# Optimization experiments

Measured on AMD Instinct MI355X. Metric: run time of the kernel, lower is better.

Reference implementation:

```python
import jax, jax.numpy as jnp
import numpy as np

M = 5  # neighbours per down point (M_i = 5 when n_up > 5)


def _per_graph(h, s_l, scores, W_emb, b_emb):
    # h: [N,H], s_l: [N,3], scores: [N]
    N, H = h.shape
    n_up = N // 4  # floor(0.25 * N)
    top_idx = jnp.argsort(-scores)[:n_up]
    up_mask = jnp.zeros((N,), bool).at[top_idx].set(True)
    up_idx = jnp.sort(top_idx)                     # up nodes in ascending node order
    down_idx = jnp.argsort(up_mask)[: N - n_up]    # stable: down nodes ascending

    # embedding_features_to_att: Linear(H+4 -> H) on concat(h, s_l, scores)
    feat = jnp.concatenate([h, s_l, scores[:, None]], axis=1) @ W_emb + b_emb  # [N,H]

    # directional KNN: for each down point, M nearest up points in 3D coords
    d2 = jnp.sum((s_l[down_idx][:, None, :] - s_l[up_idx][None, :, :]) ** 2, -1)  # [Nd,Nu]
    _, nn_local = jax.lax.top_k(-d2, M)            # [Nd,M] indices into up set
    dst = up_idx[nn_local].reshape(-1)             # edge destinations (up nodes)
    src = jnp.repeat(down_idx, M)                  # edge sources (down nodes)

    # DGL update_all: copy src 'features' -> max reduce at dst; no-msg nodes = 0
    msgs = feat[src]                               # [Nd*M, H]
    out = jnp.full((N, H), -jnp.inf, feat.dtype).at[dst].max(msgs)
    out = jnp.where(jnp.isneginf(out), jnp.zeros((), feat.dtype), out)
    return out, up_mask


def setup_inputs() -> dict:
    key = jax.random.key(0)
    k1, k2, k3, k4, k5 = jax.random.split(key, 5)
    B, N, H = 8, 8192, 256
    return {
        "h": jax.random.normal(k1, (B, N, H), jnp.float32),
        "s_l": jax.random.normal(k2, (B, N, 3), jnp.float32),
        "scores": jax.random.uniform(k3, (B, N), jnp.float32),
        "W_emb": jax.random.normal(k4, (H + 4, H), jnp.float32) * 0.02,
        "b_emb": jax.random.normal(k5, (H,), jnp.float32) * 0.02,
    }


def reference(h, s_l, scores, W_emb, b_emb):
    out, up_mask = jax.vmap(_per_graph, in_axes=(0, 0, 0, None, None))(
        h, s_l, scores, W_emb, b_emb)
    B, N, H = out.shape
    return out.reshape(B * N, H), up_mask.reshape(-1)
```

## Files before the change

kernel.cpp:

```cpp
#include <hip/hip_runtime.h>

#define Bb 8
#define Nn 8192
#define Hh 256
#define NUP 2048
#define NDOWN (Nn - NUP)
#define MM 5
#define EPB (NDOWN * MM)
#define KP 288
#define LDA 36
#define LSTW 17

typedef short v8s __attribute__((ext_vector_type(8)));
typedef float v4f __attribute__((ext_vector_type(4)));

__device__ __forceinline__ unsigned short bfc(float f) {
    unsigned u = __float_as_uint(f);
    return (unsigned short)((u + 0x7FFFu + ((u >> 16) & 1u)) >> 16);
}

template <int NB>
__device__ void find_kth_bin(const int* hist, int kth, int tid,
                             int* wsumA, int* res, int* out_bin, int* out_cntgt) {
    constexpr int PER = NB / 1024;
    int ln = tid & 63, wv = tid >> 6;
    int b0 = NB - 1 - PER * tid;
    int c0 = hist[b0];
    int c1 = (PER == 2) ? hist[b0 - 1] : 0;
    int tot = c0 + c1;
    int x = tot;
    #pragma unroll
    for (int off = 1; off < 64; off <<= 1) {
        int y = __shfl_up(x, off);
        if (ln >= off) x += y;
    }
    if (ln == 63) wsumA[wv] = x;
    __syncthreads();
    int wbase = 0;
    for (int w = 0; w < wv; w++) wbase += wsumA[w];
    int excl = wbase + x - tot;
    if (excl < kth && excl + c0 >= kth) { res[0] = b0; res[1] = excl; }
    else if (PER == 2 && excl + c0 < kth && excl + c0 + c1 >= kth) { res[0] = b0 - 1; res[1] = excl + c0; }
    __syncthreads();
    *out_bin = res[0];
    *out_cntgt = res[1];
}

__global__ __launch_bounds__(1024) void select_kernel(
        const float* __restrict__ scores, const float* __restrict__ sl,
        int* __restrict__ mask, float4* __restrict__ upc,
        float4* __restrict__ dnc, int* __restrict__ deg) {
    int b = blockIdx.x;
    int tid = threadIdx.x;
    int ln = tid & 63, wv = tid >> 6;
    __shared__ int hist[2048];
    __shared__ int wsumA[16], wsumB[16];
    __shared__ int res[2];
    __shared__ int sbase[2];
    const float* s = scores + (size_t)b * Nn;

    deg[b * NUP + tid] = 0;
    deg[b * NUP + 1024 + tid] = 0;

    hist[tid] = 0; hist[tid + 1024] = 0;
    __syncthreads();
    for (int t = tid; t < Nn; t += 1024)
        atomicAdd(&hist[__float_as_uint(s[t]) >> 21], 1);
    __syncthreads();
    int B1, gt1;
    find_kth_bin<2048>(hist, NUP, tid, wsumA, res, &B1, &gt1);
    int slots1 = NUP - gt1;

    hist[tid] = 0; hist[tid + 1024] = 0;
    __syncthreads();
    for (int t = tid; t < Nn; t += 1024) {
        unsigned u = __float_as_uint(s[t]);
        if ((int)(u >> 21) == B1) atomicAdd(&hist[(u >> 10) & 0x7FF], 1);
    }
    __syncthreads();
    int B2, gt2;
    find_kth_bin<2048>(hist, slots1, tid, wsumA, res, &B2, &gt2);
    int slots2 = slots1 - gt2;
    unsigned hi22 = ((unsigned)B1 << 11) | (unsigned)B2;

    hist[tid] = 0; hist[tid + 1024] = 0;
    __syncthreads();
    for (int t = tid; t < Nn; t += 1024) {
        unsigned u = __float_as_uint(s[t]);
        if ((u >> 10) == hi22) atomicAdd(&hist[u & 0x3FF], 1);
    }
    __syncthreads();
    int B3, gt3;
    find_kth_bin<1024>(hist, slots2, tid, wsumA, res, &B3, &gt3);
    int slots_eq = slots2 - gt3;
    unsigned T = (hi22 << 10) | (unsigned)B3;

    if (tid == 0) { sbase[0] = 0; sbase[1] = 0; }
    __syncthreads();
    for (int t0 = 0; t0 < Nn; t0 += 1024) {
        int node = t0 + tid;
        int g = b * Nn + node;
        unsigned u = __float_as_uint(s[node]);
        bool eq = (u == T);
        unsigned long long bal = __ballot(eq);
        unsigned long long lmask = (1ull << ln) - 1ull;
        int pre = __popcll(bal & lmask);
        if (ln == 0) wsumA[wv] = __popcll(bal);
        __syncthreads();
        int eqbase = sbase[0];
        for (int w = 0; w < wv; w++) eqbase += wsumA[w];
        bool up = (u > T) || (eq && (eqbase + pre) < slots_eq);
        unsigned long long bal2 = __ballot(up);
        int pre2 = __popcll(bal2 & lmask);
        if (ln == 0) wsumB[wv] = __popcll(bal2);
        __syncthreads();
        int upbase = sbase[1];
        for (int w = 0; w < wv; w++) upbase += wsumB[w];
        float4 c;
        c.x = sl[(size_t)g * 3 + 0];
        c.y = sl[(size_t)g * 3 + 1];
        c.z = sl[(size_t)g * 3 + 2];
        c.w = __int_as_float(node);
        if (up) {
            upc[b * NUP + upbase + pre2] = c;
        } else {
            dnc[b * NDOWN + node - (upbase + pre2)] = c;
        }
        mask[g] = up ? 1 : 0;
        __syncthreads();
        if (tid == 0) {
            int se = 0, su = 0;
            for (int w = 0; w < 16; w++) { se += wsumA[w]; su += wsumB[w]; }
            sbase[0] += se; sbase[1] += su;
        }
        __syncthreads();
    }
}

__global__ __launch_bounds__(512) void knn_brute(
        const float4* __restrict__ upc, const float4* __restrict__ dnc,
        int* __restrict__ knn, int* __restrict__ deg) {
    int b = blockIdx.y;
    int tid = threadIdx.x;
    int sub = tid >> 6, dn = tid & 63;
    __shared__ float xs[NUP], ys[NUP], zs[NUP];
    __shared__ unsigned long long Ubuf[1312];
    __shared__ int lcnt[64];
    float* sF = (float*)Ubuf;
    unsigned long long* lst = Ubuf + 32;

    float4 d = dnc[b * NDOWN + blockIdx.x * 64 + dn];
    float xd = d.x, yd = d.y, zd = d.z;
    int node = __float_as_int(d.w);

    const float4* U = upc + b * NUP;
    #pragma unroll
    for (int q = 0; q < 4; q++) {
        int i = q * 512 + tid;
        float4 u = U[i];
        xs[i] = u.x; ys[i] = u.y; zs[i] = u.z;
    }
    if (tid < 64) lcnt[tid] = 0;
    __syncthreads();

    float L[MM];
    #pragma unroll
    for (int m = 0; m < MM; m++) L[m] = 3.4e38f;
    const int j0 = sub * 256;
    #pragma unroll 4
    for (int j = j0; j < j0 + 256; ++j) {
        float dx = xs[j] - xd, dy = ys[j] - yd, dz = zs[j] - zd;
        float d2 = fmaf(dx, dx, fmaf(dy, dy, dz * dz));
        #pragma unroll
        for (int m = 0; m < MM; m++) {
            float lo = fminf(d2, L[m]), hi = fmaxf(d2, L[m]);
            L[m] = lo; d2 = hi;
        }
    }
    #pragma unroll
    for (int m = 0; m < MM; m++) sF[(sub * MM + m) * 64 + dn] = L[m];
    __syncthreads();

    if (sub == 0) {
        float F[MM];
        #pragma unroll
        for (int m = 0; m < MM; m++) F[m] = 3.4e38f;
        for (int l = 0; l < 8; l++) {
            #pragma unroll
            for (int m = 0; m < MM; m++) {
                float v = sF[(l * MM + m) * 64 + dn];
                #pragma unroll
                for (int k = 0; k < MM; k++) {
                    float lo = fminf(v, F[k]), hi = fmaxf(v, F[k]);
                    F[k] = lo; v = hi;
                }
            }
        }
        sF[dn] = F[MM - 1];
    }
    __syncthreads();
    float thr = sF[dn];

    #pragma unroll 4
    for (int j = j0; j < j0 + 256; ++j) {
        float dx = xs[j] - xd, dy = ys[j] - yd, dz = zs[j] - zd;
        float d2 = fmaf(dx, dx, fmaf(dy, dy, dz * dz));
        if (d2 <= thr) {
            unsigned long long key =
                ((unsigned long long)__float_as_uint(d2) << 32) |
                (unsigned long long)(unsigned)j;
            int s = atomicAdd(&lcnt[dn], 1);
            if (s < LSTW - 1) lst[dn * LSTW + s] = key;
        }
    }
    __syncthreads();

    if (sub == 0) {
        unsigned long long fin[MM];
        #pragma unroll
        for (int m = 0; m < MM; m++) fin[m] = 0xFFFFFFFFFFFFFFFFull;
        int n = min(lcnt[dn], LSTW - 1);
        for (int s = 0; s < n; s++) {
            unsigned long long cand = lst[dn * LSTW + s];
            #pragma unroll
            for (int m = 0; m < MM; m++) {
                bool lt = cand < fin[m];
                unsigned long long lo = lt ? cand : fin[m];
                unsigned long long hi = lt ? fin[m] : cand;
                fin[m] = lo; cand = hi;
            }
        }
        int g = b * Nn + node;
        #pragma unroll
        for (int m = 0; m < MM; m++) {
            int lid = (int)(unsigned)(fin[m] & 0xFFFFFFFFull);
            knn[g * MM + m] = lid;
            atomicAdd(&deg[b * NUP + lid], 1);
        }
    }
}

__global__ void wt_kernel(const float* __restrict__ W, const float* __restrict__ bias,
                          unsigned short* __restrict__ Wt) {
    int n = blockIdx.x;
    int k = threadIdx.x;
    Wt[n * KP + k] = bfc(W[(size_t)k * Hh + n]);
    if (k < KP - 256) {
        int kk = 256 + k;
        unsigned short v = 0;
        if (kk < 260)       v = bfc(W[(size_t)kk * Hh + n]);
        else if (kk == 260) v = bfc(bias[n]);
        Wt[n * KP + kk] = v;
    }
}

__global__ void feat_mfma(const float* __restrict__ h, const float* __restrict__ sl,
                          const float* __restrict__ sc, const unsigned short* __restrict__ Wt,
                          const float4* __restrict__ dnc, float* __restrict__ out) {
    int b = blockIdx.z;
    int m0 = blockIdx.x * 128;
    int n0 = blockIdx.y * 128;
    int tid = threadIdx.x;
    __shared__ unsigned short Al[128 * LDA];
    __shared__ unsigned short Bl[128 * LDA];
    __shared__ int ndid[128];
    int wid = tid >> 6, lane = tid & 63;
    int wm = (wid & 1) * 64, wn = (wid >> 1) * 64;
    int lm = lane & 15, quad = lane >> 4;
    if (tid < 128) ndid[tid] = __float_as_int(dnc[b * NDOWN + m0 + tid].w);
    v4f acc[4][4];
    #pragma unroll
    for (int i = 0; i < 4; i++)
        #pragma unroll
        for (int j = 0; j < 4; j++)
            acc[i][j] = (v4f){0.f, 0.f, 0.f, 0.f};
    const float* hb = h + (size_t)b * Nn * Hh;
    for (int t = 0; t < 9; t++) {
        int k0 = t * 32;
        __syncthreads();
        if (t < 8) {
            #pragma unroll
            for (int q = 0; q < 4; q++) {
                int e = q * 256 + tid;
                int row = e >> 3, kq = e & 7;
                float4 v = *(const float4*)(hb + (size_t)ndid[row] * Hh + k0 + kq * 4);
                ushort4 o = make_ushort4(bfc(v.x), bfc(v.y), bfc(v.z), bfc(v.w));
                *(ushort4*)(Al + row * LDA + kq * 4) = o;
            }
        } else if (tid < 128) {
            int row = tid;
            int g = b * Nn + ndid[row];
            unsigned short r[32];
            #pragma unroll
            for (int k = 0; k < 32; k++) r[k] = 0;
            r[0] = bfc(sl[(size_t)g * 3 + 0]);
            r[1] = bfc(sl[(size_t)g * 3 + 1]);
            r[2] = bfc(sl[(size_t)g * 3 + 2]);
            r[3] = bfc(sc[g]);
            r[4] = 0x3F80;
            #pragma unroll
            for (int q = 0; q < 8; q++)
                *(ushort4*)(Al + row * LDA + q * 4) =
                    make_ushort4(r[q * 4], r[q * 4 + 1], r[q * 4 + 2], r[q * 4 + 3]);
        }
        #pragma unroll
        for (int q = 0; q < 4; q++) {
            int e = q * 256 + tid;
            int n = e >> 3, kq = e & 7;
            ushort4 v = *(const ushort4*)(Wt + (size_t)(n0 + n) * KP + k0 + kq * 4);
            *(ushort4*)(Bl + n * LDA + kq * 4) = v;
        }
        __syncthreads();
        v8s af[4], bfr[4];
        #pragma unroll
        for (int i = 0; i < 4; i++)
            af[i] = *(const v8s*)(Al + (wm + i * 16 + lm) * LDA + quad * 8);
        #pragma unroll
        for (int j = 0; j < 4; j++)
            bfr[j] = *(const v8s*)(Bl + (wn + j * 16 + lm) * LDA + quad * 8);
        #pragma unroll
        for (int i = 0; i < 4; i++)
            #pragma unroll
            for (int j = 0; j < 4; j++)
                acc[i][j] = __builtin_amdgcn_mfma_f32_16x16x32_bf16(af[i], bfr[j], acc[i][j], 0, 0, 0);
    }
    #pragma unroll
    for (int i = 0; i < 4; i++) {
        #pragma unroll
        for (int r = 0; r < 4; r++) {
            int lrow = wm + i * 16 + quad * 4 + r;
            size_t base = ((size_t)b * Nn + ndid[lrow]) * Hh + n0 + wn + lm;
            #pragma unroll
            for (int j = 0; j < 4; j++)
                out[base + j * 16] = acc[i][j][r];
        }
    }
}

__global__ __launch_bounds__(1024) void csr_scan(const int* __restrict__ deg,
                                                 int* __restrict__ rowptr,
                                                 int* __restrict__ cursor) {
    int b = blockIdx.x;
    int tid = threadIdx.x;
    int ln = tid & 63, wv = tid >> 6;
    __shared__ int wsum[16];
    int d0 = deg[b * NUP + 2 * tid], d1 = deg[b * NUP + 2 * tid + 1];
    int s = d0 + d1;
    int x = s;
    #pragma unroll
    for (int off = 1; off < 64; off <<= 1) {
        int y = __shfl_up(x, off);
        if (ln >= off) x += y;
    }
    if (ln == 63) wsum[wv] = x;
    __syncthreads();
    int base = 0;
    for (int w = 0; w < wv; w++) base += wsum[w];
    int excl = base + x - s;
    rowptr[b * (NUP + 1) + 2 * tid] = excl;
    rowptr[b * (NUP + 1) + 2 * tid + 1] = excl + d0;
    cursor[b * NUP + 2 * tid] = excl;
    cursor[b * NUP + 2 * tid + 1] = excl + d0;
    if (tid == 1023) rowptr[b * (NUP + 1) + NUP] = excl + s;
}

__global__ void csr_fill(const int* __restrict__ mask, const int* __restrict__ knn,
                         int* __restrict__ cursor, int* __restrict__ edges) {
    int b = blockIdx.y;
    int i = blockIdx.x * 256 + threadIdx.x;
    int g = b * Nn + i;
    if (mask[g]) return;
    #pragma unroll
    for (int m = 0; m < MM; m++) {
        int un = knn[g * MM + m];
        int slot = atomicAdd(&cursor[b * NUP + un], 1);
        edges[b * EPB + slot] = i;
    }
}

__global__ void gather_kernel(const float4* __restrict__ upc, const int* __restrict__ rowptr,
                              const int* __restrict__ edges, float* __restrict__ out) {
    int b = blockIdx.y;
    int u = blockIdx.x * 4 + (threadIdx.x >> 6);
    int lane = threadIdx.x & 63;
    int node = __float_as_int(upc[b * NUP + u].w);
    int start = rowptr[b * (NUP + 1) + u];
    int end   = rowptr[b * (NUP + 1) + u + 1];
    const int* eb = edges + b * EPB;
    size_t rowbase = (size_t)b * Nn * Hh + (size_t)(lane << 2);
    float4 a0 = make_float4(-3.4e38f, -3.4e38f, -3.4e38f, -3.4e38f);
    float4 a1 = a0, a2 = a0, a3 = a0;
    int e = start;
    for (; e + 4 <= end; e += 4) {
        int s0 = eb[e], s1 = eb[e + 1], s2 = eb[e + 2], s3 = eb[e + 3];
        float4 v0 = *(const float4*)(out + rowbase + (size_t)s0 * Hh);
        float4 v1 = *(const float4*)(out + rowbase + (size_t)s1 * Hh);
        float4 v2 = *(const float4*)(out + rowbase + (size_t)s2 * Hh);
        float4 v3 = *(const float4*)(out + rowbase + (size_t)s3 * Hh);
        a0.x = fmaxf(a0.x, v0.x); a0.y = fmaxf(a0.y, v0.y);
        a0.z = fmaxf(a0.z, v0.z); a0.w = fmaxf(a0.w, v0.w);
        a1.x = fmaxf(a1.x, v1.x); a1.y = fmaxf(a1.y, v1.y);
        a1.z = fmaxf(a1.z, v1.z); a1.w = fmaxf(a1.w, v1.w);
        a2.x = fmaxf(a2.x, v2.x); a2.y = fmaxf(a2.y, v2.y);
        a2.z = fmaxf(a2.z, v2.z); a2.w = fmaxf(a2.w, v2.w);
        a3.x = fmaxf(a3.x, v3.x); a3.y = fmaxf(a3.y, v3.y);
        a3.z = fmaxf(a3.z, v3.z); a3.w = fmaxf(a3.w, v3.w);
    }
    for (; e < end; e++) {
        int s0 = eb[e];
        float4 v0 = *(const float4*)(out + rowbase + (size_t)s0 * Hh);
        a0.x = fmaxf(a0.x, v0.x); a0.y = fmaxf(a0.y, v0.y);
        a0.z = fmaxf(a0.z, v0.z); a0.w = fmaxf(a0.w, v0.w);
    }
    float4 r;
    r.x = fmaxf(fmaxf(a0.x, a1.x), fmaxf(a2.x, a3.x));
    r.y = fmaxf(fmaxf(a0.y, a1.y), fmaxf(a2.y, a3.y));
    r.z = fmaxf(fmaxf(a0.z, a1.z), fmaxf(a2.z, a3.z));
    r.w = fmaxf(fmaxf(a0.w, a1.w), fmaxf(a2.w, a3.w));
    if (start == end) r = make_float4(0.f, 0.f, 0.f, 0.f);
    *(float4*)(out + rowbase + (size_t)node * Hh) = r;
}

__global__ void finalize_kernel(const int* __restrict__ mask, float* __restrict__ out) {
    int b = blockIdx.y;
    int node = blockIdx.x * 4 + (threadIdx.x >> 6);
    int g = b * Nn + node;
    int lane = threadIdx.x & 63;
    bool up = mask[g] != 0;
    if (!up)
        *(float4*)(out + (size_t)g * Hh + (lane << 2)) = make_float4(0.f, 0.f, 0.f, 0.f);
    if (lane == 0) out[(size_t)Bb * Nn * Hh + g] = up ? 1.0f : 0.0f;
}

extern "C" void kernel_launch(void* const* d_in, const int* in_sizes, int n_in,
                              void* d_out, int out_size, void* d_ws, size_t ws_size,
                              hipStream_t stream) {
    const float* h    = (const float*)d_in[0];
    const float* sl   = (const float*)d_in[1];
    const float* sc   = (const float*)d_in[2];
    const float* W    = (const float*)d_in[3];
    const float* bias = (const float*)d_in[4];

    char* ws = (char*)d_ws;
    int* mask = (int*)ws;                 ws += (size_t)Bb * Nn * sizeof(int);
    int* knn  = (int*)ws;                 ws += (size_t)Bb * Nn * MM * sizeof(int);
    float4* upc = (float4*)ws;            ws += (size_t)Bb * NUP * sizeof(float4);
    float4* dnc = (float4*)ws;            ws += (size_t)Bb * NDOWN * sizeof(float4);
    unsigned short* Wt = (unsigned short*)ws; ws += (size_t)Hh * KP * sizeof(unsigned short);
    int* deg = (int*)ws;                  ws += (size_t)Bb * NUP * sizeof(int);
    int* cursor = (int*)ws;               ws += (size_t)Bb * NUP * sizeof(int);
    int* rowptr = (int*)ws;               ws += (size_t)Bb * (NUP + 1) * sizeof(int);
    int* edges = (int*)ws;
    float* outf = (float*)d_out;

    dim3 blk(256);
    select_kernel<<<dim3(Bb), dim3(1024), 0, stream>>>(sc, sl, mask, upc, dnc, deg);
    knn_brute<<<dim3(NDOWN / 64, Bb), dim3(512), 0, stream>>>(upc, dnc, knn, deg);
    csr_scan<<<dim3(Bb), dim3(1024), 0, stream>>>(deg, rowptr, cursor);
    csr_fill<<<dim3(Nn / 256, Bb), blk, 0, stream>>>(mask, knn, cursor, edges);
    wt_kernel<<<dim3(Hh), blk, 0, stream>>>(W, bias, Wt);
    feat_mfma<<<dim3(NDOWN / 128, 2, Bb), blk, 0, stream>>>(h, sl, sc, Wt, dnc, outf);
    gather_kernel<<<dim3(NUP / 4, Bb), blk, 0, stream>>>(upc, rowptr, edges, outf);
    finalize_kernel<<<dim3(Nn / 4, Bb), blk, 0, stream>>>(mask, outf);
}
```

Before: 278.9 us.

## Register-cache scores in select, use fmed3 insertion in KNN, compact csr_fill

The select kernel now has each thread load 8 contiguous scores once into registers. It builds all three histogram passes from those registers and replaces the eight-iteration ballot/barrier compaction loop with two block-wide prefix scans. The KNN top-5 insertion sort uses fmed3 instructions in place of paired min/max, which cuts the ALU ops per candidate. csr_fill launches only over down nodes, read from dnc, instead of over all nodes with a mask check. Each thread now processes contiguous nodes, so the stores to mask and sl are less coalesced.

After: 264.5 us. 5.2% less time.

```diff
diff --git a/kernel.cpp b/kernel.cpp
--- a/kernel.cpp
+++ b/kernel.cpp
@@ -54,18 +54,24 @@
     int tid = threadIdx.x;
     int ln = tid & 63, wv = tid >> 6;
     __shared__ int hist[2048];
-    __shared__ int wsumA[16], wsumB[16];
+    __shared__ int wsumA[16];
     __shared__ int res[2];
-    __shared__ int sbase[2];
     const float* s = scores + (size_t)b * Nn;
 
     deg[b * NUP + tid] = 0;
     deg[b * NUP + 1024 + tid] = 0;
 
+    float4 sa = *(const float4*)(s + tid * 8);
+    float4 sb = *(const float4*)(s + tid * 8 + 4);
+    unsigned ub[8] = {__float_as_uint(sa.x), __float_as_uint(sa.y),
+                      __float_as_uint(sa.z), __float_as_uint(sa.w),
+                      __float_as_uint(sb.x), __float_as_uint(sb.y),
+                      __float_as_uint(sb.z), __float_as_uint(sb.w)};
+
     hist[tid] = 0; hist[tid + 1024] = 0;
     __syncthreads();
-    for (int t = tid; t < Nn; t += 1024)
-        atomicAdd(&hist[__float_as_uint(s[t]) >> 21], 1);
+    #pragma unroll
+    for (int k = 0; k < 8; k++) atomicAdd(&hist[ub[k] >> 21], 1);
     __syncthreads();
     int B1, gt1;
     find_kth_bin<2048>(hist, NUP, tid, wsumA, res, &B1, &gt1);
@@ -73,10 +79,9 @@
 
     hist[tid] = 0; hist[tid + 1024] = 0;
     __syncthreads();
-    for (int t = tid; t < Nn; t += 1024) {
-        unsigned u = __float_as_uint(s[t]);
-        if ((int)(u >> 21) == B1) atomicAdd(&hist[(u >> 10) & 0x7FF], 1);
-    }
+    #pragma unroll
+    for (int k = 0; k < 8; k++)
+        if ((int)(ub[k] >> 21) == B1) atomicAdd(&hist[(ub[k] >> 10) & 0x7FF], 1);
     __syncthreads();
     int B2, gt2;
     find_kth_bin<2048>(hist, slots1, tid, wsumA, res, &B2, &gt2);
@@ -85,55 +90,65 @@
 
     hist[tid] = 0; hist[tid + 1024] = 0;
     __syncthreads();
-    for (int t = tid; t < Nn; t += 1024) {
-        unsigned u = __float_as_uint(s[t]);
-        if ((u >> 10) == hi22) atomicAdd(&hist[u & 0x3FF], 1);
-    }
+    #pragma unroll
+    for (int k = 0; k < 8; k++)
+        if ((ub[k] >> 10) == hi22) atomicAdd(&hist[ub[k] & 0x3FF], 1);
     __syncthreads();
     int B3, gt3;
     find_kth_bin<1024>(hist, slots2, tid, wsumA, res, &B3, &gt3);
     int slots_eq = slots2 - gt3;
     unsigned T = (hi22 << 10) | (unsigned)B3;
 
-    if (tid == 0) { sbase[0] = 0; sbase[1] = 0; }
-    __syncthreads();
-    for (int t0 = 0; t0 < Nn; t0 += 1024) {
-        int node = t0 + tid;
+    int eqc = 0;
+    #pragma unroll
+    for (int k = 0; k < 8; k++) eqc += (ub[k] == T) ? 1 : 0;
+    int x = eqc;
+    #pragma unroll
+    for (int off = 1; off < 64; off <<= 1) {
+        int y = __shfl_up(x, off);
+        if (ln >= off) x += y;
+    }
+    if (ln == 63) wsumA[wv] = x;
+    __syncthreads();
+    int eqb = x - eqc;
+    for (int w = 0; w < wv; w++) eqb += wsumA[w];
+    __syncthreads();
+
+    int upcnt = 0, eqrun = 0, upf = 0;
+    #pragma unroll
+    for (int k = 0; k < 8; k++) {
+        bool eq = (ub[k] == T);
+        bool up = (ub[k] > T) || (eq && (eqb + eqrun) < slots_eq);
+        eqrun += eq ? 1 : 0;
+        upf |= (up ? 1 : 0) << k;
+        upcnt += up ? 1 : 0;
+    }
+    x = upcnt;
+    #pragma unroll
+    for (int off = 1; off < 64; off <<= 1) {
+        int y = __shfl_up(x, off);
+        if (ln >= off) x += y;
+    }
+    if (ln == 63) wsumA[wv] = x;
+    __syncthreads();
+    int upb = x - upcnt;
+    for (int w = 0; w < wv; w++) upb += wsumA[w];
+
+    int uprun = 0;
+    #pragma unroll
+    for (int k = 0; k < 8; k++) {
+        int node = tid * 8 + k;
         int g = b * Nn + node;
-        unsigned u = __float_as_uint(s[node]);
-        bool eq = (u == T);
-        unsigned long long bal = __ballot(eq);
-        unsigned long long lmask = (1ull << ln) - 1ull;
-        int pre = __popcll(bal & lmask);
-        if (ln == 0) wsumA[wv] = __popcll(bal);
-        __syncthreads();
-        int eqbase = sbase[0];
-        for (int w = 0; w < wv; w++) eqbase += wsumA[w];
-        bool up = (u > T) || (eq && (eqbase + pre) < slots_eq);
-        unsigned long long bal2 = __ballot(up);
-        int pre2 = __popcll(bal2 & lmask);
-        if (ln == 0) wsumB[wv] = __popcll(bal2);
-        __syncthreads();
-        int upbase = sbase[1];
-        for (int w = 0; w < wv; w++) upbase += wsumB[w];
         float4 c;
         c.x = sl[(size_t)g * 3 + 0];
         c.y = sl[(size_t)g * 3 + 1];
         c.z = sl[(size_t)g * 3 + 2];
         c.w = __int_as_float(node);
-        if (up) {
-            upc[b * NUP + upbase + pre2] = c;
-        } else {
-            dnc[b * NDOWN + node - (upbase + pre2)] = c;
-        }
+        bool up = (upf >> k) & 1;
+        if (up) upc[b * NUP + upb + uprun] = c;
+        else    dnc[b * NDOWN + node - (upb + uprun)] = c;
         mask[g] = up ? 1 : 0;
-        __syncthreads();
-        if (tid == 0) {
-            int se = 0, su = 0;
-            for (int w = 0; w < 16; w++) { se += wsumA[w]; su += wsumB[w]; }
-            sbase[0] += se; sbase[1] += su;
-        }
-        __syncthreads();
+        uprun += up ? 1 : 0;
     }
 }
 
@@ -163,40 +178,39 @@
     if (tid < 64) lcnt[tid] = 0;
     __syncthreads();
 
-    float L[MM];
-    #pragma unroll
-    for (int m = 0; m < MM; m++) L[m] = 3.4e38f;
+    float L0 = 3.4e38f, L1 = 3.4e38f, L2 = 3.4e38f, L3 = 3.4e38f, L4 = 3.4e38f;
     const int j0 = sub * 256;
     #pragma unroll 4
     for (int j = j0; j < j0 + 256; ++j) {
         float dx = xs[j] - xd, dy = ys[j] - yd, dz = zs[j] - zd;
         float d2 = fmaf(dx, dx, fmaf(dy, dy, dz * dz));
-        #pragma unroll
-        for (int m = 0; m < MM; m++) {
-            float lo = fminf(d2, L[m]), hi = fmaxf(d2, L[m]);
-            L[m] = lo; d2 = hi;
-        }
-    }
-    #pragma unroll
-    for (int m = 0; m < MM; m++) sF[(sub * MM + m) * 64 + dn] = L[m];
+        L4 = __builtin_amdgcn_fmed3f(d2, L3, L4);
+        L3 = __builtin_amdgcn_fmed3f(d2, L2, L3);
+        L2 = __builtin_amdgcn_fmed3f(d2, L1, L2);
+        L1 = __builtin_amdgcn_fmed3f(d2, L0, L1);
+        L0 = fminf(d2, L0);
+    }
+    sF[(sub * MM + 0) * 64 + dn] = L0;
+    sF[(sub * MM + 1) * 64 + dn] = L1;
+    sF[(sub * MM + 2) * 64 + dn] = L2;
+    sF[(sub * MM + 3) * 64 + dn] = L3;
+    sF[(sub * MM + 4) * 64 + dn] = L4;
     __syncthreads();
 
     if (sub == 0) {
-        float F[MM];
-        #pragma unroll
-        for (int m = 0; m < MM; m++) F[m] = 3.4e38f;
+        float F0 = 3.4e38f, F1 = 3.4e38f, F2 = 3.4e38f, F3 = 3.4e38f, F4 = 3.4e38f;
         for (int l = 0; l < 8; l++) {
             #pragma unroll
             for (int m = 0; m < MM; m++) {
                 float v = sF[(l * MM + m) * 64 + dn];
-                #pragma unroll
-                for (int k = 0; k < MM; k++) {
-                    float lo = fminf(v, F[k]), hi = fmaxf(v, F[k]);
-                    F[k] = lo; v = hi;
-                }
+                F4 = __builtin_amdgcn_fmed3f(v, F3, F4);
+                F3 = __builtin_amdgcn_fmed3f(v, F2, F3);
+                F2 = __builtin_amdgcn_fmed3f(v, F1, F2);
+                F1 = __builtin_amdgcn_fmed3f(v, F0, F1);
+                F0 = fminf(v, F0);
             }
         }
-        sF[dn] = F[MM - 1];
+        sF[dn] = F4;
     }
     __syncthreads();
     float thr = sF[dn];
@@ -364,17 +378,17 @@
     if (tid == 1023) rowptr[b * (NUP + 1) + NUP] = excl + s;
 }
 
-__global__ void csr_fill(const int* __restrict__ mask, const int* __restrict__ knn,
+__global__ void csr_fill(const float4* __restrict__ dnc, const int* __restrict__ knn,
                          int* __restrict__ cursor, int* __restrict__ edges) {
     int b = blockIdx.y;
-    int i = blockIdx.x * 256 + threadIdx.x;
-    int g = b * Nn + i;
-    if (mask[g]) return;
+    int r = blockIdx.x * 256 + threadIdx.x;
+    int node = __float_as_int(dnc[b * NDOWN + r].w);
+    int g = b * Nn + node;
     #pragma unroll
     for (int m = 0; m < MM; m++) {
         int un = knn[g * MM + m];
         int slot = atomicAdd(&cursor[b * NUP + un], 1);
-        edges[b * EPB + slot] = i;
+        edges[b * EPB + slot] = node;
     }
 }
 
@@ -457,7 +471,7 @@
     select_kernel<<<dim3(Bb), dim3(1024), 0, stream>>>(sc, sl, mask, upc, dnc, deg);
     knn_brute<<<dim3(NDOWN / 64, Bb), dim3(512), 0, stream>>>(upc, dnc, knn, deg);
     csr_scan<<<dim3(Bb), dim3(1024), 0, stream>>>(deg, rowptr, cursor);
-    csr_fill<<<dim3(Nn / 256, Bb), blk, 0, stream>>>(mask, knn, cursor, edges);
+    csr_fill<<<dim3(NDOWN / 256, Bb), blk, 0, stream>>>(dnc, knn, cursor, edges);
     wt_kernel<<<dim3(Hh), blk, 0, stream>>>(W, bias, Wt);
     feat_mfma<<<dim3(NDOWN / 128, 2, Bb), blk, 0, stream>>>(h, sl, sc, Wt, dnc, outf);
     gather_kernel<<<dim3(NUP / 4, Bb), blk, 0, stream>>>(upc, rowptr, edges, outf);
```
